# Optimization experiments

Hardware: AMD Instinct MI355X
Metric: run time of the kernel (lower is better)

## Reference

```python
import jax, jax.numpy as jnp
import numpy as np

TEMP = 0.07


def setup_inputs() -> dict:
    key = jax.random.key(0)
    kq, kk = jax.random.split(key)
    B, D = 8192, 128
    q = jax.random.normal(kq, (B, D), dtype=jnp.float32)
    k = jax.random.normal(kk, (B, D), dtype=jnp.float32)
    return {"q": q, "k": k}


def reference(q, k):
    # features = cat([q, k], dim=0); F.normalize(dim=1)
    B = q.shape[0]
    N = 2 * B
    f = jnp.concatenate([q, k], axis=0)
    f = f / jnp.maximum(jnp.linalg.norm(f, axis=1, keepdims=True), 1e-12)
    sim = f @ f.T  # [N, N]

    i = jnp.arange(N)
    p = (i + B) % N                      # index of the positive pair of row i
    pos = sim[i, p][:, None]             # [N, 1]

    # negatives: all columns except the diagonal (i) and the positive (p),
    # in original column order (matches boolean-mask ordering in torch).
    a = jnp.minimum(i, p)[:, None]       # [N, 1]
    b = jnp.maximum(i, p)[:, None]
    j = jnp.arange(N - 2)[None, :]       # [1, N-2]
    c = j + (j >= a)                     # skip first excluded column
    c = c + (c >= b)                     # skip second excluded column
    neg = jnp.take_along_axis(sim, c, axis=1)  # [N, N-2]

    logits = jnp.concatenate([pos, neg], axis=1) / TEMP  # [N, N-1]
    labels = jnp.zeros((N,), dtype=jnp.int32)
    return logits, labels
```

## Files before the change

### kernel.cpp

```cpp
#include <hip/hip_runtime.h>
#include <hip/hip_bf16.h>
#include <stdint.h>

#define B_ROWS 8192
#define N_TOT  16384
#define D_DIM  128
#define SCALE_SQRT_INVT 3.7796447300922722f

typedef __bf16 bf16x8 __attribute__((ext_vector_type(8)));
typedef float  f32x4  __attribute__((ext_vector_type(4)));

__global__ void simclr_norm_kernel(const float* __restrict__ q,
                                   const float* __restrict__ k,
                                   unsigned int* __restrict__ fb) {
    const int lane = threadIdx.x & 63;
    const int row  = blockIdx.x * 4 + (threadIdx.x >> 6);
    const float* src = (row < B_ROWS) ? (q + (size_t)row * D_DIM)
                                      : (k + (size_t)(row - B_ROWS) * D_DIM);
    float2 v = ((const float2*)src)[lane];
    float s = v.x * v.x + v.y * v.y;
#pragma unroll
    for (int off = 32; off > 0; off >>= 1) s += __shfl_xor(s, off);
    float rn = SCALE_SQRT_INVT / fmaxf(sqrtf(s), 1e-12f);
    union { __bf16 h[2]; unsigned int u; } pk;
    pk.h[0] = (__bf16)(v.x * rn);
    pk.h[1] = (__bf16)(v.y * rn);
    fb[(size_t)row * 64 + lane] = pk.u;
}

__global__ __launch_bounds__(256, 2) void simclr_gemm_kernel(
        const unsigned short* __restrict__ fb, float* __restrict__ out) {
    __shared__ char lds[32768];

    const int bid = blockIdx.x;
    const int r0  = (bid >> 1) * 64;
    const int h   = bid & 1;
    const int tid  = threadIdx.x;
    const int lane = tid & 63;
    const int w    = tid >> 6;
    const int rl = lane & 15;
    const int kg = lane >> 4;

    const char* fbb = (const char*)fb;

    bf16x8 afr[4][4];
#pragma unroll
    for (int m = 0; m < 4; ++m)
#pragma unroll
        for (int ks = 0; ks < 4; ++ks)
            afr[m][ks] = *(const bf16x8*)(fbb + (size_t)(r0 + m * 16 + rl) * 256 + ks * 64 + kg * 16);

    for (int t = 0; t < 64; ++t) {
        const int c0 = h * 8192 + t * 128;

#pragma unroll
        for (int rnd = 0; rnd < 8; ++rnd) {
            const int row   = rnd * 16 + w * 4 + (lane >> 4);
            const int chunk = (lane & 15) ^ (row & 7);
            const char* g = fbb + (size_t)(c0 + row) * 256 + chunk * 16;
            char* l = lds + (rnd * 16 + w * 4) * 256;
            __builtin_amdgcn_global_load_lds((const __attribute__((address_space(1))) void*)g,
                                             (__attribute__((address_space(3))) void*)l, 16, 0, 0);
        }
        __syncthreads();

        f32x4 acc[4][2];
#pragma unroll
        for (int m = 0; m < 4; ++m)
#pragma unroll
            for (int n = 0; n < 2; ++n) acc[m][n] = (f32x4){0.f, 0.f, 0.f, 0.f};

#pragma unroll
        for (int ks = 0; ks < 4; ++ks) {
            const int kb = ks * 64 + kg * 16;
            bf16x8 bfr[2];
#pragma unroll
            for (int n = 0; n < 2; ++n) {
                const int rr = w * 32 + n * 16 + rl;
                bfr[n] = *(const bf16x8*)(lds + rr * 256 + (kb ^ ((rr & 7) << 4)));
            }
#pragma unroll
            for (int m = 0; m < 4; ++m)
#pragma unroll
                for (int n = 0; n < 2; ++n)
                    acc[m][n] = __builtin_amdgcn_mfma_f32_16x16x32_bf16(bfr[n], afr[m][ks], acc[m][n], 0, 0, 0);
        }

        const int cw = c0 + w * 32 + (kg << 2);
#pragma unroll
        for (int m = 0; m < 4; ++m) {
            const int i = r0 + m * 16 + rl;
            const int p = i ^ B_ROWS;
            const int a = i & (B_ROWS - 1);
            const int b = a | B_ROWS;
            float* orow = out + (size_t)i * (N_TOT - 1);
#pragma unroll
            for (int n = 0; n < 2; ++n) {
                const int c = cw + n * 16;
                f32x4 v = acc[m][n];
                if (__builtin_expect((unsigned)(a - c) < 4u || (unsigned)(b - c) < 4u, 0)) {
#pragma unroll
                    for (int e = 0; e < 4; ++e) {
                        const int cc = c + e;
                        const float val = v[e];
                        if (cc == i) continue;
                        if (cc == p) { orow[0] = val; continue; }
                        orow[cc + 1 - (cc > a) - (cc > b)] = val;
                    }
                } else {
                    const int s = 1 - (c > a) - (c > b);
                    __builtin_memcpy(orow + c + s, &v, sizeof(v));
                }
            }
        }
        __syncthreads();
    }
}

__global__ void simclr_zero_labels(float* __restrict__ out) {
    out[(size_t)N_TOT * (N_TOT - 1) + blockIdx.x * 256 + threadIdx.x] = 0.0f;
}

extern "C" void kernel_launch(void* const* d_in, const int* in_sizes, int n_in,
                              void* d_out, int out_size, void* d_ws, size_t ws_size,
                              hipStream_t stream) {
    const float* q = (const float*)d_in[0];
    const float* k = (const float*)d_in[1];
    float* out = (float*)d_out;
    unsigned int* fb = (unsigned int*)d_ws;

    simclr_norm_kernel<<<N_TOT / 4, 256, 0, stream>>>(q, k, fb);
    simclr_zero_labels<<<N_TOT / 256, 256, 0, stream>>>(out);
    simclr_gemm_kernel<<<512, 256, 0, stream>>>((const unsigned short*)d_ws, out);
}
```

Baseline: 405.2 us.

## Double-buffer LDS tiles with async prefetch of next column block

Doubles the LDS allocation so the next 128-column tile is fetched with global_load_lds while the current tile is consumed. Synchronisation switches from `__syncthreads` to manual `s_waitcnt vmcnt` plus `s_barrier`. All B fragments are read into registers before a second barrier, which lets the trailing barrier after the output stores be dropped. The aim is to hide load latency and let output stores overlap the next iteration. In exchange the kernel uses more LDS and depends on hand-counted vmcnt values, which also count outstanding stores.

```diff
diff --git a/kernel.cpp b/kernel.cpp
--- a/kernel.cpp
+++ b/kernel.cpp
@@ -30,7 +30,7 @@
 
 __global__ __launch_bounds__(256, 2) void simclr_gemm_kernel(
         const unsigned short* __restrict__ fb, float* __restrict__ out) {
-    __shared__ char lds[32768];
+    __shared__ char lds[65536];
 
     const int bid = blockIdx.x;
     const int r0  = (bid >> 1) * 64;
@@ -43,6 +43,21 @@
 
     const char* fbb = (const char*)fb;
 
+    auto stage = [&](int buf, int t) {
+        const int c0 = h * 8192 + t * 128;
+#pragma unroll
+        for (int rnd = 0; rnd < 8; ++rnd) {
+            const int row   = rnd * 16 + w * 4 + (lane >> 4);
+            const int chunk = (lane & 15) ^ (row & 7);
+            const char* g = fbb + (size_t)(c0 + row) * 256 + chunk * 16;
+            char* l = lds + buf * 32768 + (rnd * 16 + w * 4) * 256;
+            __builtin_amdgcn_global_load_lds((const __attribute__((address_space(1))) void*)g,
+                                             (__attribute__((address_space(3))) void*)l, 16, 0, 0);
+        }
+    };
+
+    stage(0, 0);
+
     bf16x8 afr[4][4];
 #pragma unroll
     for (int m = 0; m < 4; ++m)
@@ -51,41 +66,47 @@
             afr[m][ks] = *(const bf16x8*)(fbb + (size_t)(r0 + m * 16 + rl) * 256 + ks * 64 + kg * 16);
 
     for (int t = 0; t < 64; ++t) {
-        const int c0 = h * 8192 + t * 128;
+        const int cur = t & 1;
 
+        if (t < 63) {
+            stage(cur ^ 1, t + 1);
+            asm volatile("s_waitcnt vmcnt(16)" ::: "memory");
+        } else {
+            asm volatile("s_waitcnt vmcnt(8)" ::: "memory");
+        }
+        __builtin_amdgcn_sched_barrier(0);
+        __builtin_amdgcn_s_barrier();
+        __builtin_amdgcn_sched_barrier(0);
+
+        bf16x8 bfr[4][2];
 #pragma unroll
-        for (int rnd = 0; rnd < 8; ++rnd) {
-            const int row   = rnd * 16 + w * 4 + (lane >> 4);
-            const int chunk = (lane & 15) ^ (row & 7);
-            const char* g = fbb + (size_t)(c0 + row) * 256 + chunk * 16;
-            char* l = lds + (rnd * 16 + w * 4) * 256;
-            __builtin_amdgcn_global_load_lds((const __attribute__((address_space(1))) void*)g,
-                                             (__attribute__((address_space(3))) void*)l, 16, 0, 0);
+        for (int ks = 0; ks < 4; ++ks) {
+            const int kb = ks * 64 + kg * 16;
+#pragma unroll
+            for (int n = 0; n < 2; ++n) {
+                const int rr = w * 32 + n * 16 + rl;
+                bfr[ks][n] = *(const bf16x8*)(lds + cur * 32768 + rr * 256 + (kb ^ ((rr & 7) << 4)));
+            }
         }
-        __syncthreads();
+        asm volatile("s_waitcnt lgkmcnt(0)" ::: "memory");
+        __builtin_amdgcn_sched_barrier(0);
+        __builtin_amdgcn_s_barrier();
+        __builtin_amdgcn_sched_barrier(0);
 
         f32x4 acc[4][2];
 #pragma unroll
         for (int m = 0; m < 4; ++m)
 #pragma unroll
             for (int n = 0; n < 2; ++n) acc[m][n] = (f32x4){0.f, 0.f, 0.f, 0.f};
-
 #pragma unroll
-        for (int ks = 0; ks < 4; ++ks) {
-            const int kb = ks * 64 + kg * 16;
-            bf16x8 bfr[2];
-#pragma unroll
-            for (int n = 0; n < 2; ++n) {
-                const int rr = w * 32 + n * 16 + rl;
-                bfr[n] = *(const bf16x8*)(lds + rr * 256 + (kb ^ ((rr & 7) << 4)));
-            }
+        for (int ks = 0; ks < 4; ++ks)
 #pragma unroll
             for (int m = 0; m < 4; ++m)
 #pragma unroll
                 for (int n = 0; n < 2; ++n)
-                    acc[m][n] = __builtin_amdgcn_mfma_f32_16x16x32_bf16(bfr[n], afr[m][ks], acc[m][n], 0, 0, 0);
-        }
+                    acc[m][n] = __builtin_amdgcn_mfma_f32_16x16x32_bf16(bfr[ks][n], afr[m][ks], acc[m][n], 0, 0, 0);
 
+        const int c0 = h * 8192 + t * 128;
         const int cw = c0 + w * 32 + (kg << 2);
 #pragma unroll
         for (int m = 0; m < 4; ++m) {
@@ -113,7 +134,6 @@
                 }
             }
         }
-        __syncthreads();
     }
 }
 
```

Result: faster. 360.5 us (-11.0%).
